# Kernel optimization log

Measured on AMD Instinct MI355X. Metric: run time of the kernel, lower is better.

## Reference

```python
import jax, jax.numpy as jnp
import numpy as np

N_NODES = 100000
N_EDGES = 1600000
D_FEAT = 64


def setup_inputs() -> dict:
    key = jax.random.key(0)
    k1, k2, k3, k4 = jax.random.split(key, 4)
    row = jnp.sort(jax.random.randint(k1, (N_EDGES,), 0, N_NODES, dtype=jnp.int32))
    col = jax.random.randint(k2, (N_EDGES,), 0, N_NODES, dtype=jnp.int32)
    values = jax.random.uniform(k3, (N_EDGES,), dtype=jnp.float32)
    x = jax.random.normal(k4, (N_NODES, D_FEAT), dtype=jnp.float32)
    return {"row": row, "col": col, "values": values, "x": x}


def reference(row, col, values, x):
    # spmm_scatter: out[row[e]] += values[e] * x[col[e]]  (gather-multiply-scatter)
    msgs = x[col] * values[:, None]                      # [E, d]
    out = jax.ops.segment_sum(msgs, row, num_segments=x.shape[0])  # [N, d]
    return out
```

## Files before the change

### kernel.cpp

```cpp
#include <hip/hip_runtime.h>
#include <hip/hip_fp16.h>


constexpr int D   = 64;
constexpr int DV  = 16;
constexpr int DH8 = 8;

struct __align__(16) h8 { __half2 a, b, c, d; };

__global__ __launch_bounds__(256) void prep_kernel(
    const int* __restrict__ row,
    const float4* __restrict__ x4,
    h8* __restrict__ xh,
    int* __restrict__ row_ptr,
    int nEdges, int n8, int nNodes)
{
    const int i = blockIdx.x * blockDim.x + threadIdx.x;
    if (i < n8) {
        const float4 lo = x4[2 * i];
        const float4 hi = x4[2 * i + 1];
        h8 h;
        h.a = __float22half2_rn(make_float2(lo.x, lo.y));
        h.b = __float22half2_rn(make_float2(lo.z, lo.w));
        h.c = __float22half2_rn(make_float2(hi.x, hi.y));
        h.d = __float22half2_rn(make_float2(hi.z, hi.w));
        xh[i] = h;
    }
    if (i < nEdges) {
        const int r    = row[i];
        const int prev = (i == 0) ? -1 : row[i - 1];
        for (int n = prev + 1; n <= r; ++n) row_ptr[n] = i;
        if (i == nEdges - 1)
            for (int n = r + 1; n <= nNodes; ++n) row_ptr[n] = nEdges;
    }
}

__device__ __forceinline__ void fma_h8(const h8& p, float v, float4& a0, float4& a1)
{
    float2 f;
    f = __half22float2(p.a); a0.x = fmaf(v, f.x, a0.x); a0.y = fmaf(v, f.y, a0.y);
    f = __half22float2(p.b); a0.z = fmaf(v, f.x, a0.z); a0.w = fmaf(v, f.y, a0.w);
    f = __half22float2(p.c); a1.x = fmaf(v, f.x, a1.x); a1.y = fmaf(v, f.y, a1.y);
    f = __half22float2(p.d); a1.z = fmaf(v, f.x, a1.z); a1.w = fmaf(v, f.y, a1.w);
}

__global__ __launch_bounds__(256) void spmm_h8(
    const int* __restrict__ row_ptr,
    const int* __restrict__ col,
    const float* __restrict__ val,
    const h8* __restrict__ xh,
    float4* __restrict__ out4,
    int nNodes)
{
    const int wid = (blockIdx.x * blockDim.x + threadIdx.x) >> 6;
    if (wid >= nNodes) return;
    const int lane = threadIdx.x & 63;
    const int g    = lane >> 3;
    const int sub  = lane & 7;

    const int uw    = __builtin_amdgcn_readfirstlane(wid);
    const int start = row_ptr[uw];
    const int end   = row_ptr[uw + 1];
    const int deg   = end - start;

    const int  eL  = start + lane;
    const bool okL = eL < end;
    const int   cv = okL ? col[eL] : 0;
    const float vv = okL ? val[eL] : 0.f;

    float4 a0 = {0.f, 0.f, 0.f, 0.f};
    float4 a1 = {0.f, 0.f, 0.f, 0.f};

    const int it64 = min((deg + 15) >> 4, 4);
    for (int it = 0; it < it64; ++it) {
        const int s0 = it * 16 + 2 * g;
        const int   c0 = __shfl(cv, s0, 64);
        const float v0 = __shfl(vv, s0, 64);
        const int   c1 = __shfl(cv, s0 + 1, 64);
        const float v1 = __shfl(vv, s0 + 1, 64);
        const h8 p0 = xh[(size_t)c0 * DH8 + sub];
        const h8 p1 = xh[(size_t)c1 * DH8 + sub];
        fma_h8(p0, v0, a0, a1);
        fma_h8(p1, v1, a0, a1);
    }

    for (int ebase = start + 64; ebase < end; ebase += 16) {
        const int e0 = ebase + 2 * g, e1 = e0 + 1;
        int c0 = 0, c1 = 0; float v0 = 0.f, v1 = 0.f;
        if (e0 < end) { c0 = col[e0]; v0 = val[e0]; }
        if (e1 < end) { c1 = col[e1]; v1 = val[e1]; }
        const h8 p0 = xh[(size_t)c0 * DH8 + sub];
        const h8 p1 = xh[(size_t)c1 * DH8 + sub];
        fma_h8(p0, v0, a0, a1);
        fma_h8(p1, v1, a0, a1);
    }

    #pragma unroll
    for (int off = 8; off <= 32; off <<= 1) {
        a0.x += __shfl_xor(a0.x, off, 64); a0.y += __shfl_xor(a0.y, off, 64);
        a0.z += __shfl_xor(a0.z, off, 64); a0.w += __shfl_xor(a0.w, off, 64);
        a1.x += __shfl_xor(a1.x, off, 64); a1.y += __shfl_xor(a1.y, off, 64);
        a1.z += __shfl_xor(a1.z, off, 64); a1.w += __shfl_xor(a1.w, off, 64);
    }
    if (g == 0) {
        out4[(size_t)wid * DV + 2 * sub]     = a0;
        out4[(size_t)wid * DV + 2 * sub + 1] = a1;
    }
}

__global__ __launch_bounds__(256) void spmm_psearch(
    const int* __restrict__ row,
    const int* __restrict__ col,
    const float* __restrict__ val,
    const float4* __restrict__ x4,
    float4* __restrict__ out4,
    int nEdges, int nNodes)
{
    const int wid = (blockIdx.x * blockDim.x + threadIdx.x) >> 6;
    if (wid >= nNodes) return;
    const int lane  = threadIdx.x & 63;
    const int group = lane >> 4;
    const int sub   = lane & 15;

    int lo = 0, hi = nEdges;
    const int t0 = wid;
    while (hi > lo) {
        const int span = hi - lo + 1;
        if (span <= 64) {
            const int idx = lo + lane;
            const bool lt = (idx <= hi) && (idx < nEdges) && (row[idx] < t0);
            lo += __popcll(__ballot(lt));
            break;
        }
        const int step = (span + 63) >> 6;
        const int idx  = lo + lane * step;
        const bool lt  = (idx <= hi) && (idx < nEdges) && (row[idx] < t0);
        const int  c   = __popcll(__ballot(lt));
        if (c == 0) { hi = lo; break; }
        const int new_lo = lo + (c - 1) * step + 1;
        if (c < 64) hi = lo + c * step;
        lo = new_lo;
    }
    const int start = lo;
    const int t1 = wid + 1;
    int end = start;
    for (;;) {
        const int idx = end + lane;
        const bool lt = (idx < nEdges) && (row[idx] < t1);
        const int  c  = __popcll(__ballot(lt));
        end += c;
        if (c < 64) break;
    }

    float4 acc = {0.f, 0.f, 0.f, 0.f};
    for (int e = start + group; e < end; e += 8) {
        const int e1 = e + 4;
        const int   c0 = col[e];
        const float v0 = val[e];
        int c1 = c0; float v1 = 0.f;
        if (e1 < end) { c1 = col[e1]; v1 = val[e1]; }
        const float4 x0 = x4[(size_t)c0 * DV + sub];
        const float4 x1 = x4[(size_t)c1 * DV + sub];
        acc.x = fmaf(v0, x0.x, acc.x); acc.y = fmaf(v0, x0.y, acc.y);
        acc.z = fmaf(v0, x0.z, acc.z); acc.w = fmaf(v0, x0.w, acc.w);
        acc.x = fmaf(v1, x1.x, acc.x); acc.y = fmaf(v1, x1.y, acc.y);
        acc.z = fmaf(v1, x1.z, acc.z); acc.w = fmaf(v1, x1.w, acc.w);
    }
    #pragma unroll
    for (int off = 16; off <= 32; off <<= 1) {
        acc.x += __shfl_xor(acc.x, off, 64);
        acc.y += __shfl_xor(acc.y, off, 64);
        acc.z += __shfl_xor(acc.z, off, 64);
        acc.w += __shfl_xor(acc.w, off, 64);
    }
    if (group == 0) out4[(size_t)wid * DV + sub] = acc;
}

extern "C" void kernel_launch(void* const* d_in, const int* in_sizes, int n_in,
                              void* d_out, int out_size, void* d_ws, size_t ws_size,
                              hipStream_t stream)
{
    const int*    row  = (const int*)   d_in[0];
    const int*    col  = (const int*)   d_in[1];
    const float*  val  = (const float*) d_in[2];
    const float4* x4   = (const float4*)d_in[3];
    float4*       out4 = (float4*)d_out;

    const int nEdges = in_sizes[0];
    const int nNodes = out_size / D;
    const int n8     = nNodes * DH8;

    const dim3 block(256);
    const dim3 gridMain(((size_t)nNodes * 64 + 255) / 256);

    const size_t rp_bytes = (size_t)(nNodes + 1) * sizeof(int);
    const size_t xh_off   = (rp_bytes + 255) & ~(size_t)255;
    const size_t need     = xh_off + (size_t)nNodes * D * sizeof(__half);

    if (ws_size >= need) {
        int* row_ptr = (int*)d_ws;
        h8*  xh      = (h8*)((char*)d_ws + xh_off);
        const int prep_n = (nEdges > n8) ? nEdges : n8;
        prep_kernel<<<dim3((prep_n + 255) / 256), block, 0, stream>>>(
            row, x4, xh, row_ptr, nEdges, n8, nNodes);
        spmm_h8<<<gridMain, block, 0, stream>>>(
            row_ptr, col, val, xh, out4, nNodes);
    } else {
        spmm_psearch<<<gridMain, block, 0, stream>>>(
            row, col, val, x4, out4, nEdges, nNodes);
    }
}
```

Before: 124.5 us.

## Process two rows per wavefront in half-precision SpMM kernel

Each 64-lane wavefront now handles two consecutive rows, one per 32-lane half, instead of one. With an average degree of 16, a single row left most of the 64-edge load slot and the 16-edge inner step underused, so packing two rows is meant to cut idle lanes and halve the wavefront count. In exchange, each group of 8 lanes now processes one edge per iteration instead of two, which lowers memory-level parallelism per lane. The loop length is set by the larger of the two degrees, and the output path adds a shuffle-based transpose.

```diff
diff --git a/kernel.cpp b/kernel.cpp
--- a/kernel.cpp
+++ b/kernel.cpp
@@ -44,68 +44,84 @@
     f = __half22float2(p.d); a1.z = fmaf(v, f.x, a1.z); a1.w = fmaf(v, f.y, a1.w);
 }
 
-__global__ __launch_bounds__(256) void spmm_h8(
+__global__ __launch_bounds__(256) void spmm_h8x2(
     const int* __restrict__ row_ptr,
     const int* __restrict__ col,
     const float* __restrict__ val,
     const h8* __restrict__ xh,
     float4* __restrict__ out4,
-    int nNodes)
-{
-    const int wid = (blockIdx.x * blockDim.x + threadIdx.x) >> 6;
-    if (wid >= nNodes) return;
+    int nPairs, int nNodes)
+{
+    const int pw = (blockIdx.x * blockDim.x + threadIdx.x) >> 6;
+    if (pw >= nPairs) return;
     const int lane = threadIdx.x & 63;
-    const int g    = lane >> 3;
+    const int half = lane >> 5;
+    const int g    = (lane >> 3) & 3;
     const int sub  = lane & 7;
 
-    const int uw    = __builtin_amdgcn_readfirstlane(wid);
-    const int start = row_ptr[uw];
-    const int end   = row_ptr[uw + 1];
-    const int deg   = end - start;
-
-    const int  eL  = start + lane;
-    const bool okL = eL < end;
-    const int   cv = okL ? col[eL] : 0;
-    const float vv = okL ? val[eL] : 0.f;
+    const int upw = __builtin_amdgcn_readfirstlane(pw);
+    const int n0  = upw * 2;
+    const bool has1 = (n0 + 1) < nNodes;
+
+    const int s0 = row_ptr[n0];
+    const int s1 = row_ptr[n0 + 1];
+    const int s2 = has1 ? row_ptr[n0 + 2] : s1;
+    const int d0 = s1 - s0;
+    const int d1 = s2 - s1;
+    const int span = s2 - s0;
 
     float4 a0 = {0.f, 0.f, 0.f, 0.f};
     float4 a1 = {0.f, 0.f, 0.f, 0.f};
 
-    const int it64 = min((deg + 15) >> 4, 4);
-    for (int it = 0; it < it64; ++it) {
-        const int s0 = it * 16 + 2 * g;
-        const int   c0 = __shfl(cv, s0, 64);
-        const float v0 = __shfl(vv, s0, 64);
-        const int   c1 = __shfl(cv, s0 + 1, 64);
-        const float v1 = __shfl(vv, s0 + 1, 64);
-        const h8 p0 = xh[(size_t)c0 * DH8 + sub];
-        const h8 p1 = xh[(size_t)c1 * DH8 + sub];
-        fma_h8(p0, v0, a0, a1);
-        fma_h8(p1, v1, a0, a1);
-    }
-
-    for (int ebase = start + 64; ebase < end; ebase += 16) {
-        const int e0 = ebase + 2 * g, e1 = e0 + 1;
-        int c0 = 0, c1 = 0; float v0 = 0.f, v1 = 0.f;
-        if (e0 < end) { c0 = col[e0]; v0 = val[e0]; }
-        if (e1 < end) { c1 = col[e1]; v1 = val[e1]; }
-        const h8 p0 = xh[(size_t)c0 * DH8 + sub];
-        const h8 p1 = xh[(size_t)c1 * DH8 + sub];
-        fma_h8(p0, v0, a0, a1);
-        fma_h8(p1, v1, a0, a1);
+    if (span <= 64) {
+        const int  eL  = s0 + lane;
+        const bool okL = eL < s2;
+        const int   cv = okL ? col[eL] : 0;
+        const float vv = okL ? val[eL] : 0.f;
+
+        const int bh    = half ? d0 : 0;
+        const int degh  = half ? d1 : d0;
+        const int itmax = (max(d0, d1) + 3) >> 2;
+        for (int it = 0; it < itmax; ++it) {
+            const int  sl   = it * 4 + g;
+            const bool ok   = sl < degh;
+            const int  slot = min(bh + (ok ? sl : 0), 63);
+            const int   c = __shfl(cv, slot, 64);
+            float       v = __shfl(vv, slot, 64);
+            v = ok ? v : 0.f;
+            const h8 p = xh[(size_t)c * DH8 + sub];
+            fma_h8(p, v, a0, a1);
+        }
+    } else {
+        const int bs = half ? s1 : s0;
+        const int be = half ? s2 : s1;
+        for (int e = bs + g; e < be; e += 4) {
+            const int   c = col[e];
+            const float v = val[e];
+            const h8 p = xh[(size_t)c * DH8 + sub];
+            fma_h8(p, v, a0, a1);
+        }
     }
 
     #pragma unroll
-    for (int off = 8; off <= 32; off <<= 1) {
+    for (int off = 8; off <= 16; off <<= 1) {
         a0.x += __shfl_xor(a0.x, off, 64); a0.y += __shfl_xor(a0.y, off, 64);
         a0.z += __shfl_xor(a0.z, off, 64); a0.w += __shfl_xor(a0.w, off, 64);
         a1.x += __shfl_xor(a1.x, off, 64); a1.y += __shfl_xor(a1.y, off, 64);
         a1.z += __shfl_xor(a1.z, off, 64); a1.w += __shfl_xor(a1.w, off, 64);
     }
-    if (g == 0) {
-        out4[(size_t)wid * DV + 2 * sub]     = a0;
-        out4[(size_t)wid * DV + 2 * sub + 1] = a1;
-    }
+
+    const int t   = lane & 31;
+    const int src = (lane & 32) + (t >> 1);
+    float4 b0, b1;
+    b0.x = __shfl(a0.x, src, 64); b0.y = __shfl(a0.y, src, 64);
+    b0.z = __shfl(a0.z, src, 64); b0.w = __shfl(a0.w, src, 64);
+    b1.x = __shfl(a1.x, src, 64); b1.y = __shfl(a1.y, src, 64);
+    b1.z = __shfl(a1.z, src, 64); b1.w = __shfl(a1.w, src, 64);
+    const float4 r = (t & 1) ? b1 : b0;
+    const int node = n0 + half;
+    if (t < 16 && node < nNodes)
+        out4[(size_t)node * DV + t] = r;
 }
 
 __global__ __launch_bounds__(256) void spmm_psearch(
@@ -189,9 +205,9 @@
     const int nEdges = in_sizes[0];
     const int nNodes = out_size / D;
     const int n8     = nNodes * DH8;
+    const int nPairs = (nNodes + 1) / 2;
 
     const dim3 block(256);
-    const dim3 gridMain(((size_t)nNodes * 64 + 255) / 256);
 
     const size_t rp_bytes = (size_t)(nNodes + 1) * sizeof(int);
     const size_t xh_off   = (rp_bytes + 255) & ~(size_t)255;
@@ -203,10 +219,10 @@
         const int prep_n = (nEdges > n8) ? nEdges : n8;
         prep_kernel<<<dim3((prep_n + 255) / 256), block, 0, stream>>>(
             row, x4, xh, row_ptr, nEdges, n8, nNodes);
-        spmm_h8<<<gridMain, block, 0, stream>>>(
-            row_ptr, col, val, xh, out4, nNodes);
+        spmm_h8x2<<<dim3(((size_t)nPairs * 64 + 255) / 256), block, 0, stream>>>(
+            row_ptr, col, val, xh, out4, nPairs, nNodes);
     } else {
-        spmm_psearch<<<gridMain, block, 0, stream>>>(
+        spmm_psearch<<<dim3(((size_t)nNodes * 64 + 255) / 256), block, 0, stream>>>(
             row, col, val, x4, out4, nEdges, nNodes);
     }
 }
```

Measured after the change: 123.3 us, median of 2. No clear change (-1.0%).
